# Kernel optimization log

Measured on AMD Instinct MI355X. Metric: run time of the kernel, lower is better.

Reference implementation:

```python
import jax, jax.numpy as jnp
import numpy as np

DN = ('NCHW', 'OIHW', 'NCHW')

def conv2d(x, w, b):
    y = jax.lax.conv_general_dilated(x, w, window_strides=(1, 1), padding='VALID', dimension_numbers=DN)
    return y + b[None, :, None, None]

def setup_inputs() -> dict:
    key = jax.random.key(0)
    ks = jax.random.split(key, 16)
    s = 0.02  # small init scale to keep relu chains numerically tame
    B, Cin, OUT = 128, 4, 9
    return {
        'state_m': jax.random.normal(ks[0], (B, Cin, 100, 100), jnp.float32),
        'state_g': jax.random.normal(ks[1], (B, 2), jnp.float32),
        'state_v': jax.random.normal(ks[2], (B, 2), jnp.float32),
        'conv1_w': jax.random.normal(ks[3], (32, Cin, 32, 32), jnp.float32) * s,
        'conv1_b': jnp.zeros((32,), jnp.float32),
        'conv2_w': jax.random.normal(ks[4], (64, 32, 32, 32), jnp.float32) * s,
        'conv2_b': jnp.zeros((64,), jnp.float32),
        'conv3_w': jax.random.normal(ks[5], (64, 64, 8, 8), jnp.float32) * s,
        'conv3_b': jnp.zeros((64,), jnp.float32),
        'conv4_w': jax.random.normal(ks[6], (64, 64, 8, 8), jnp.float32) * s,
        'conv4_b': jnp.zeros((64,), jnp.float32),
        'fc1_w': jax.random.normal(ks[7], (67, 4), jnp.float32) * s,
        'fc1_b': jnp.zeros((67,), jnp.float32),
        'fc2_w': jax.random.normal(ks[8], (512, 6400), jnp.float32) * s,
        'fc2_b': jnp.zeros((512,), jnp.float32),
        'fc3_w': jax.random.normal(ks[9], (512, 512), jnp.float32) * s,
        'fc3_b': jnp.zeros((512,), jnp.float32),
        'fc4_ea_w': jax.random.normal(ks[10], (OUT, 512), jnp.float32) * s,
        'fc4_ea_b': jnp.zeros((OUT,), jnp.float32),
        'fc4_ev_w': jax.random.normal(ks[11], (1, 512), jnp.float32) * s,
        'fc4_ev_b': jnp.zeros((1,), jnp.float32),
    }

def reference(state_m, state_g, state_v,
              conv1_w, conv1_b, conv2_w, conv2_b, conv3_w, conv3_b, conv4_w, conv4_b,
              fc1_w, fc1_b, fc2_w, fc2_b, fc3_w, fc3_b,
              fc4_ea_w, fc4_ea_b, fc4_ev_w, fc4_ev_b):
    x_m = jax.nn.relu(conv2d(state_m, conv1_w, conv1_b))   # [B,32,69,69]
    x_m = jax.nn.relu(conv2d(x_m, conv2_w, conv2_b))       # [B,64,38,38]
    x_m = jax.nn.relu(conv2d(x_m, conv3_w, conv3_b))       # [B,64,31,31]
    x_gv_ = jax.nn.relu(jnp.concatenate([state_g, state_v], axis=1) @ fc1_w.T + fc1_b)  # [B,67]
    convw = x_m.shape[2]  # 31
    # Torch loop overwrites x_gv each iteration: final tile is filled with x_gv_[0, convw-1]
    scalar = x_gv_[0, convw - 1]
    x_pls = x_m + scalar  # broadcast add (the CPU round-trip tile in torch)
    x_pls = jax.nn.relu(conv2d(x_pls, conv4_w, conv4_b))   # [B,64,24,24]
    x_pls = jax.nn.relu(conv2d(x_pls, conv4_w, conv4_b))   # [B,64,17,17]
    x_pls = jax.nn.relu(conv2d(x_pls, conv4_w, conv4_b))   # [B,64,10,10]
    x = x_pls.reshape(x_pls.shape[0], -1)                  # [B,6400]
    x = jax.nn.relu(x @ fc2_w.T + fc2_b)
    x = jax.nn.relu(x @ fc3_w.T + fc3_b)
    adv = x @ fc4_ea_w.T + fc4_ea_b                        # [B,outputs]
    val = x @ fc4_ev_w.T + fc4_ev_b                        # [B,1]
    return adv + val - jnp.mean(adv, axis=1, keepdims=True)
```

## Files before the change

kernel.cpp:

```cpp
#include <hip/hip_runtime.h>
#include <stdint.h>


using bf16_t = __bf16;
using bf16x8 = __attribute__((ext_vector_type(8))) __bf16;
using bf16x4 = __attribute__((ext_vector_type(4))) __bf16;
using f32x4  = __attribute__((ext_vector_type(4))) float;
using f32x16 = __attribute__((ext_vector_type(16))) float;

__device__ __forceinline__ f32x4 mfma16(bf16x8 a, bf16x8 b, f32x4 c) {
    return __builtin_amdgcn_mfma_f32_16x16x32_bf16(a, b, c, 0, 0, 0);
}
__device__ __forceinline__ f32x16 mfma32(bf16x8 a, bf16x8 b, f32x16 c) {
    return __builtin_amdgcn_mfma_f32_32x32x16_bf16(a, b, c, 0, 0, 0);
}

template<bool A16>
__device__ __forceinline__ bf16x8 load_frag(const bf16_t* p) {
    if constexpr (A16) {
        return *reinterpret_cast<const bf16x8*>(p);
    } else {
        union { bf16x8 v; uint64_t u[2]; } r;
        r.u[0] = *reinterpret_cast<const uint64_t*>(p);
        r.u[1] = *reinterpret_cast<const uint64_t*>(p + 4);
        return r.v;
    }
}

template<int CIN>
__global__ void pack_w(const float* __restrict__ src, bf16_t* __restrict__ dst,
                       int COUT, int KK) {
    int total = COUT * KK;
    for (int t = blockIdx.x * blockDim.x + threadIdx.x; t < total;
         t += gridDim.x * blockDim.x) {
        int cout = t / KK;
        int khw  = t - cout * KK;
        alignas(16) bf16_t tmp[CIN];
        #pragma unroll
        for (int c = 0; c < CIN; ++c)
            tmp[c] = (bf16_t)src[((size_t)cout * CIN + c) * KK + khw];
        bf16_t* d = dst + (size_t)t * CIN;
        if constexpr (CIN == 1) {
            d[0] = tmp[0];
        } else if constexpr (CIN == 4) {
            *reinterpret_cast<uint2*>(d) = *reinterpret_cast<const uint2*>(tmp);
        } else {
            #pragma unroll
            for (int c = 0; c < CIN; c += 8)
                *reinterpret_cast<uint4*>(d + c) =
                    *reinterpret_cast<const uint4*>(tmp + c);
        }
    }
}

template<int CIN, int COUT, int K>
__global__ void pack_wA(const float* __restrict__ src, bf16_t* __restrict__ dst) {
    constexpr int S  = K * CIN / 16;
    constexpr int NT = COUT / 32;
    int t = blockIdx.x * 256 + threadIdx.x;
    int l  = t & 63;
    int f  = t >> 6;
    int n  = f % NT;
    int fs = f / NT;
    int s  = fs % S;
    int kh = fs / S;
    if (kh >= K) return;
    int cout = n * 32 + (l & 31);
    int k0   = s * 16 + (l >> 5) * 8;
    alignas(16) bf16_t tmp[8];
    #pragma unroll
    for (int e = 0; e < 8; ++e) {
        int k   = k0 + e;
        int kw  = k / CIN;
        int cin = k % CIN;
        tmp[e] = (bf16_t)src[(((size_t)cout * CIN + cin) * K + kh) * K + kw];
    }
    *reinterpret_cast<uint4*>(dst + (size_t)t * 8) =
        *reinterpret_cast<const uint4*>(tmp);
}

__global__ void fc1_scalar(const float* __restrict__ g, const float* __restrict__ v,
                           const float* __restrict__ w, const float* __restrict__ b,
                           float* __restrict__ outp) {
    if (threadIdx.x == 0 && blockIdx.x == 0) {
        float s = b[30] + g[0] * w[120] + g[1] * w[121] + v[0] * w[122] + v[1] * w[123];
        *outp = s > 0.f ? s : 0.f;
    }
}

__global__ __launch_bounds__(256, 2) void conv2_k4(
    const bf16_t* __restrict__ in, const bf16_t* __restrict__ wA,
    const float* __restrict__ bias, bf16_t* __restrict__ out) {
    constexpr int W = 69, OW = 38, CIN = 32;
    constexpr int P    = OW * OW;
    constexpr int ROWB = W * CIN * 2;
    constexpr int PS   = (W + 1) * 16;
    constexpr int SLOTB = 4576;
    constexpr int NSLOT = 16;
    constexpr int LDSB  = NSLOT * SLOTB;
    constexpr int S = 64, NT = 2, WMT = 3;
    constexpr int BPX = 384;
    constexpr int CHR = ROWB / 16;
    constexpr int CH4 = 4 * CHR;
    __shared__ __align__(16) char smem[LDSB];

    const int tid  = threadIdx.x;
    const int wave = tid >> 6, lane = tid & 63;
    const int l31  = lane & 31, h = lane >> 5;
    const int img  = blockIdx.z;
    const int p0   = blockIdx.x * BPX;

    const char* inb = (const char*)(in + (size_t)img * (W * W * CIN));
    const int r0 = p0 / OW;
    int plast = p0 + BPX - 1; if (plast > P - 1) plast = P - 1;
    const int r1 = plast / OW;

    int pix[WMT], ldsadr[WMT];
    #pragma unroll
    for (int m = 0; m < WMT; ++m) {
        int p  = p0 + (wave * WMT + m) * 32 + l31;
        pix[m] = p;
        int pc = p < P ? p : P - 1;
        int oh = pc / OW;
        int ow = pc - oh * OW;
        ldsadr[m] = (oh & 15) * SLOTB + ow * 16 + h * PS;
    }

    for (int r = r0; r <= r1 + 3; ++r) {
        const char* g = inb + (size_t)r * ROWB;
        int base = (r & 15) * SLOTB;
        for (int c = tid; c < CHR; c += 256)
            *reinterpret_cast<bf16x8*>(smem + base + (c & 3) * PS + (c >> 2) * 16) =
                *reinterpret_cast<const bf16x8*>(g + c * 16);
    }
    __syncthreads();

    f32x16 acc[WMT][NT] = {};
    int wsl = (r1 + 4) & 15;
    const char* gpre = inb + (size_t)(r1 + 4) * ROWB;
    const bf16_t* wl = wA + lane * 8;

    for (int kp = 0; kp < 8; ++kp) {
        const bool pf = kp < 7;
        bf16x8 stv[5];

#define STVISSUE                                                            \
        if (pf) {                                                           \
            _Pragma("unroll")                                               \
            for (int i = 0; i < 5; ++i) {                                   \
                int c = i * 256 + tid;                                      \
                if (c < CH4) stv[i] = *reinterpret_cast<const bf16x8*>(gpre + c * 16); \
            }                                                               \
        }

        #pragma unroll
        for (int kl = 0; kl < 4; ++kl) {
            const bf16_t* ap = wl + (size_t)(kp * 4 + kl) * (S * NT * 512);
            int adr[WMT];
            #pragma unroll
            for (int m = 0; m < WMT; ++m) {
                int a = ldsadr[m] + kl * SLOTB;
                adr[m] = a >= LDSB ? a - LDSB : a;
            }

            bf16x8 bS0[WMT], bS1[WMT], bS2[WMT], bS3[WMT];
            bf16x8 aS0[NT],  aS1[NT],  aS2[NT],  aS3[NT];

#define LOADSET(BS, AS, SIDX)                                               \
            {                                                               \
                const int _s = (SIDX);                                      \
                _Pragma("unroll")                                           \
                for (int m = 0; m < WMT; ++m)                               \
                    BS[m] = *reinterpret_cast<const bf16x8*>(                \
                        smem + adr[m] + (_s & 1) * (2 * PS) + (_s >> 1) * 16); \
                _Pragma("unroll")                                           \
                for (int n = 0; n < NT; ++n)                                \
                    AS[n] = *reinterpret_cast<const bf16x8*>(ap + (_s * NT + n) * 512); \
            }
#define MFMASET(BS, AS)                                                     \
            {                                                               \
                __builtin_amdgcn_s_setprio(1);                              \
                _Pragma("unroll")                                           \
                for (int m = 0; m < WMT; ++m)                               \
                    _Pragma("unroll")                                       \
                    for (int n = 0; n < NT; ++n)                            \
                        acc[m][n] = mfma32(AS[n], BS[m], acc[m][n]);        \
                __builtin_amdgcn_s_setprio(0);                              \
            }

            LOADSET(bS0, aS0, 0)
            LOADSET(bS1, aS1, 1)
            LOADSET(bS2, aS2, 2)
            MFMASET(bS0, aS0)  LOADSET(bS3, aS3, 3)
            MFMASET(bS1, aS1)  LOADSET(bS0, aS0, 4)
            MFMASET(bS2, aS2)  LOADSET(bS1, aS1, 5)
            MFMASET(bS3, aS3)  LOADSET(bS2, aS2, 6)
            if (kl == 0) { STVISSUE }
            for (int sb = 4; sb + 8 <= S; sb += 4) {
                MFMASET(bS0, aS0)  LOADSET(bS3, aS3, sb + 3)
                MFMASET(bS1, aS1)  LOADSET(bS0, aS0, sb + 4)
                MFMASET(bS2, aS2)  LOADSET(bS1, aS1, sb + 5)
                MFMASET(bS3, aS3)  LOADSET(bS2, aS2, sb + 6)
            }
            MFMASET(bS0, aS0)  LOADSET(bS3, aS3, S - 1)
            MFMASET(bS1, aS1)
            MFMASET(bS2, aS2)
            MFMASET(bS3, aS3)
#undef LOADSET
#undef MFMASET
        }
#undef STVISSUE

        if (pf) {
            #pragma unroll
            for (int i = 0; i < 5; ++i) {
                int c = i * 256 + tid;
                if (c < CH4) {
                    int j = c / CHR, u = c - j * CHR;
                    *reinterpret_cast<bf16x8*>(
                        smem + ((wsl + j) & 15) * SLOTB + (u & 3) * PS + (u >> 2) * 16) = stv[i];
                }
            }
            gpre += 4 * ROWB;
            wsl = (wsl + 4) & 15;
        }
        __syncthreads();
        #pragma unroll
        for (int m = 0; m < WMT; ++m) {
            int a2 = ldsadr[m] + 4 * SLOTB;
            ldsadr[m] = a2 >= LDSB ? a2 - LDSB : a2;
        }
    }

    bf16_t* outb = out + (size_t)img * ((size_t)P * 64);
    #pragma unroll
    for (int m = 0; m < WMT; ++m) {
        if (pix[m] < P) {
            #pragma unroll
            for (int n = 0; n < NT; ++n) {
                #pragma unroll
                for (int rg = 0; rg < 4; ++rg) {
                    int cb = n * 32 + rg * 8 + h * 4;
                    f32x4 bv = *reinterpret_cast<const f32x4*>(bias + cb);
                    union { bf16x4 v; uint2 u; } o;
                    #pragma unroll
                    for (int j = 0; j < 4; ++j) {
                        float x = acc[m][n][rg * 4 + j] + bv[j];
                        o.v[j] = (bf16_t)(x > 0.f ? x : 0.f);
                    }
                    *reinterpret_cast<uint2*>(outb + (size_t)pix[m] * 64 + cb) = o.u;
                }
            }
        }
    }
}

template<int CIN, int COUT, int W, int K, int OW, int WMT, int NSLOT,
         int ADD_SCALAR>
__global__ __launch_bounds__(256, 2) void conv_rr(
    const bf16_t* __restrict__ in, const bf16_t* __restrict__ wA,
    const float* __restrict__ bias, bf16_t* __restrict__ out,
    const float* __restrict__ scal) {
    constexpr int  P     = OW * OW;
    constexpr int  PIXB  = CIN * 2;
    constexpr int  ROWB  = W * PIXB;
    constexpr bool TR    = (CIN >= 16);
    constexpr int  NCH   = TR ? PIXB / 16 : 1;
    constexpr int  SPP   = TR ? NCH / 2 : 1;
    constexpr int  PS    = TR ? (W + 1) * 16 : 0;
    constexpr int  SLOTB0 = TR ? NCH * PS : ROWB;
    constexpr int  PADB  = TR ? ((16 * OW - SLOTB0) % 128 + 128) % 128 : 0;
    constexpr int  SLOTB = SLOTB0 + PADB;
    constexpr int  LDSB  = NSLOT * SLOTB;
    constexpr int  S     = K * CIN / 16;
    constexpr int  NT    = COUT / 32;
    constexpr int  BPX   = WMT * 32 * 4;
    constexpr int  CH    = ROWB / 16;
    constexpr int  NLD   = (CH + 255) / 256;
    __shared__ __align__(16) char smem[LDSB];

    const int tid  = threadIdx.x;
    const int wave = tid >> 6, lane = tid & 63;
    const int l31  = lane & 31, h = lane >> 5;
    const int img  = blockIdx.z;
    const int p0   = blockIdx.x * BPX;

    const char* inb = (const char*)(in + (size_t)img * ((size_t)W * W * CIN));

    const int r0 = p0 / OW;
    int plast = p0 + BPX - 1; if (plast > P - 1) plast = P - 1;
    const int r1 = plast / OW;

    int woff[NLD];
    #pragma unroll
    for (int i = 0; i < NLD; ++i) {
        int c = i * 256 + tid;
        if (c < CH) woff[i] = TR ? (c % NCH) * PS + (c / NCH) * 16 : c * 16;
        else        woff[i] = 0;
    }

    int pix[WMT], ldsadr[WMT];
    #pragma unroll
    for (int m = 0; m < WMT; ++m) {
        int p  = p0 + (wave * WMT + m) * 32 + l31;
        pix[m] = p;
        int pc = p < P ? p : P - 1;
        int oh = pc / OW;
        int ow = pc - oh * OW;
        ldsadr[m] = (oh % NSLOT) * SLOTB +
                    (TR ? ow * 16 + h * PS : ow * PIXB + h * 16);
    }

    for (int r = r0; r <= r1; ++r) {
        const char* g = inb + (size_t)r * ROWB;
        int base = (r % NSLOT) * SLOTB;
        for (int c = tid; c < CH; c += 256) {
            bf16x8 v = *reinterpret_cast<const bf16x8*>(g + c * 16);
            int off = TR ? (c % NCH) * PS + (c / NCH) * 16 : c * 16;
            *reinterpret_cast<bf16x8*>(smem + base + off) = v;
        }
    }
    __syncthreads();

    f32x16 acc[WMT][NT] = {};

    int wsl = (r1 + 1) % NSLOT;
    const char* gpre = inb + (size_t)(r1 + 1) * ROWB;
    const bf16_t* wl = wA + lane * 8;

    for (int kh = 0; kh < K; ++kh) {
        bf16x8 stv[NLD];
        const bool pf = kh < K - 1;
        const bf16_t* ap = wl + (size_t)kh * (S * NT * 512);

        auto bread = [&](int m, int s) -> bf16x8 {
            int a = TR ? ldsadr[m] + (s % SPP) * (2 * PS) + (s / SPP) * 16
                       : ldsadr[m] + s * 32;
            return *reinterpret_cast<const bf16x8*>(smem + a);
        };
        bf16x8 bcur[WMT], acur[NT];
        #pragma unroll
        for (int m = 0; m < WMT; ++m) bcur[m] = bread(m, 0);
        #pragma unroll
        for (int n = 0; n < NT; ++n)
            acur[n] = *reinterpret_cast<const bf16x8*>(ap + n * 512);

        #pragma unroll
        for (int s = 0; s < S - 1; ++s) {
            bf16x8 bnx[WMT], anx[NT];
            #pragma unroll
            for (int m = 0; m < WMT; ++m) bnx[m] = bread(m, s + 1);
            #pragma unroll
            for (int n = 0; n < NT; ++n)
                anx[n] = *reinterpret_cast<const bf16x8*>(ap + ((s + 1) * NT + n) * 512);
            if (s == 2 && pf) {
                #pragma unroll
                for (int i = 0; i < NLD; ++i) {
                    int c = i * 256 + tid;
                    if (c < CH) stv[i] = *reinterpret_cast<const bf16x8*>(gpre + c * 16);
                }
            }
            #pragma unroll
            for (int m = 0; m < WMT; ++m)
                #pragma unroll
                for (int n = 0; n < NT; ++n)
                    acc[m][n] = mfma32(acur[n], bcur[m], acc[m][n]);
            #pragma unroll
            for (int m = 0; m < WMT; ++m) bcur[m] = bnx[m];
            #pragma unroll
            for (int n = 0; n < NT; ++n) acur[n] = anx[n];
        }
        #pragma unroll
        for (int m = 0; m < WMT; ++m)
            #pragma unroll
            for (int n = 0; n < NT; ++n)
                acc[m][n] = mfma32(acur[n], bcur[m], acc[m][n]);

        if (pf) {
            int wb0 = wsl * SLOTB;
            #pragma unroll
            for (int i = 0; i < NLD; ++i) {
                int c = i * 256 + tid;
                if (c < CH)
                    *reinterpret_cast<bf16x8*>(smem + wb0 + woff[i]) = stv[i];
            }
            gpre += ROWB;
            wsl = (wsl + 1 == NSLOT) ? 0 : wsl + 1;
        }
        __syncthreads();
        #pragma unroll
        for (int m = 0; m < WMT; ++m) {
            int a2 = ldsadr[m] + SLOTB;
            ldsadr[m] = a2 >= LDSB ? a2 - LDSB : a2;
        }
    }

    float sc = 0.f;
    if constexpr (ADD_SCALAR) sc = *scal;
    bf16_t* outb = out + (size_t)img * ((size_t)P * COUT);
    #pragma unroll
    for (int m = 0; m < WMT; ++m) {
        if (pix[m] < P) {
            #pragma unroll
            for (int n = 0; n < NT; ++n) {
                #pragma unroll
                for (int rg = 0; rg < 4; ++rg) {
                    int cb = n * 32 + rg * 8 + h * 4;
                    f32x4 bv = *reinterpret_cast<const f32x4*>(bias + cb);
                    union { bf16x4 v; uint2 u; } o;
                    #pragma unroll
                    for (int j = 0; j < 4; ++j) {
                        float x = acc[m][n][rg * 4 + j] + bv[j];
                        x = x > 0.f ? x : 0.f;
                        x += sc;
                        o.v[j] = (bf16_t)x;
                    }
                    *reinterpret_cast<uint2*>(outb + (size_t)pix[m] * COUT + cb) = o.u;
                }
            }
        }
    }
}

template<int CIN, int COUT, int W, int K, int OW, int NBLK, int WMT,
         int ADD_SCALAR, bool A16>
__global__ __launch_bounds__(256, 2) void conv_mfma(
    const bf16_t* __restrict__ in, const bf16_t* __restrict__ wp,
    const float* __restrict__ bias, bf16_t* __restrict__ out,
    const float* __restrict__ scal) {
    constexpr int P    = OW * OW;
    constexpr int KCIN = K * CIN;
    constexpr int KTOT = K * KCIN;
    constexpr int RS   = KCIN / 32;
    constexpr int NT   = NBLK / 16;
    constexpr int BMT  = WMT * 4;

    const int b     = blockIdx.z;
    const int cout0 = blockIdx.y * NBLK;
    const int wave  = threadIdx.x >> 6;
    const int lane  = threadIdx.x & 63;
    const int l15   = lane & 15;
    const int l4    = lane >> 4;
    const int mt0   = blockIdx.x * BMT + wave * WMT;

    const bf16_t* inb = in + (size_t)b * (W * W * CIN);

    int      pix[WMT];
    uint32_t pb[WMT];
    #pragma unroll
    for (int m = 0; m < WMT; ++m) {
        int p  = (mt0 + m) * 16 + l15;
        pix[m] = p;
        int pc = p < P ? p : P - 1;
        int oh = pc / OW;
        int ow = pc - oh * OW;
        pb[m]  = (uint32_t)(oh * W + ow) * CIN;
    }
    uint32_t wb[NT];
    #pragma unroll
    for (int n = 0; n < NT; ++n)
        wb[n] = (uint32_t)(cout0 + n * 16 + l15) * KTOT + (uint32_t)l4 * 8u;

    f32x4 acc[WMT][NT];
    #pragma unroll
    for (int m = 0; m < WMT; ++m)
        #pragma unroll
        for (int n = 0; n < NT; ++n)
            acc[m][n] = f32x4{0.f, 0.f, 0.f, 0.f};

    uint32_t bofs = (uint32_t)l4 * 8u;
    for (int kh = 0; kh < K; ++kh) {
        #pragma unroll
        for (int s = 0; s < RS; ++s) {
            bf16x8 af[NT];
            #pragma unroll
            for (int n = 0; n < NT; ++n)
                af[n] = load_frag<true>(wp + wb[n] + kh * KCIN + s * 32);
            #pragma unroll
            for (int m = 0; m < WMT; ++m) {
                bf16x8 bfr = load_frag<A16>(inb + pb[m] + bofs + s * 32);
                #pragma unroll
                for (int n = 0; n < NT; ++n)
                    acc[m][n] = mfma16(af[n], bfr, acc[m][n]);
            }
        }
        bofs += (uint32_t)(W * CIN);
    }

    float sc = 0.f;
    if constexpr (ADD_SCALAR) sc = *scal;
    bf16_t* outb = out + (size_t)b * P * COUT;
    #pragma unroll
    for (int n = 0; n < NT; ++n) {
        const int cb = cout0 + n * 16 + l4 * 4;
        f32x4 bv = *reinterpret_cast<const f32x4*>(bias + cb);
        #pragma unroll
        for (int m = 0; m < WMT; ++m) {
            if (pix[m] < P) {
                f32x4 v = acc[m][n];
                union { bf16x4 h; uint2 u; } st;
                #pragma unroll
                for (int r = 0; r < 4; ++r) {
                    float x = v[r] + bv[r];
                    x = x > 0.f ? x : 0.f;
                    x += sc;
                    st.h[r] = (bf16_t)x;
                }
                *reinterpret_cast<uint2*>(outb + (size_t)pix[m] * COUT + cb) = st.u;
            }
        }
    }
}

__global__ __launch_bounds__(256, 2) void fc2_kernel(
    const bf16_t* __restrict__ x, const bf16_t* __restrict__ w,
    float* __restrict__ part) {
    const int nb = blockIdx.x, kc = blockIdx.y;
    const int wave = threadIdx.x >> 6, lane = threadIdx.x & 63;
    const int l15 = lane & 15, l4 = lane >> 4;
    const int wm = wave & 1, wn = wave >> 1;

    f32x4 acc[4][2];
    #pragma unroll
    for (int m = 0; m < 4; ++m)
        #pragma unroll
        for (int n = 0; n < 2; ++n) acc[m][n] = f32x4{0.f, 0.f, 0.f, 0.f};

    uint32_t xb[4], wbf[2];
    #pragma unroll
    for (int m = 0; m < 4; ++m)
        xb[m] = (uint32_t)(16 * (wm * 4 + m) + l15) * 6400u + kc * 1600u + l4 * 8u;
    #pragma unroll
    for (int n = 0; n < 2; ++n)
        wbf[n] = (uint32_t)(nb * 64 + wn * 32 + n * 16 + l15) * 6400u + kc * 1600u + l4 * 8u;

    for (int s = 0; s < 50; ++s) {
        bf16x8 af[2];
        #pragma unroll
        for (int n = 0; n < 2; ++n)
            af[n] = load_frag<true>(w + wbf[n] + s * 32);
        #pragma unroll
        for (int m = 0; m < 4; ++m) {
            bf16x8 bfr = load_frag<true>(x + xb[m] + s * 32);
            #pragma unroll
            for (int n = 0; n < 2; ++n)
                acc[m][n] = mfma16(af[n], bfr, acc[m][n]);
        }
    }
    #pragma unroll
    for (int m = 0; m < 4; ++m) {
        int bcol = 16 * (wm * 4 + m) + l15;
        #pragma unroll
        for (int n = 0; n < 2; ++n) {
            int cf = nb * 64 + wn * 32 + n * 16 + l4 * 4;
            *reinterpret_cast<f32x4*>(part + ((size_t)kc * 128 + bcol) * 512 + cf) =
                acc[m][n];
        }
    }
}

__global__ void fc2_reduce(const float* __restrict__ part,
                           const float* __restrict__ bias,
                           bf16_t* __restrict__ xo) {
    int t = blockIdx.x * 256 + threadIdx.x;
    if (t < 128 * 512) {
        int b = t >> 9, co = t & 511;
        float s = bias[co];
        #pragma unroll
        for (int kc = 0; kc < 4; ++kc) s += part[((size_t)kc * 128 + b) * 512 + co];
        xo[t] = (bf16_t)(s > 0.f ? s : 0.f);
    }
}

__global__ __launch_bounds__(256, 2) void fc3_kernel(
    const bf16_t* __restrict__ x, const bf16_t* __restrict__ w,
    const float* __restrict__ bias, bf16_t* __restrict__ xo) {
    const int nb = blockIdx.x;
    const int wave = threadIdx.x >> 6, lane = threadIdx.x & 63;
    const int l15 = lane & 15, l4 = lane >> 4;

    f32x4 acc[2][4];
    #pragma unroll
    for (int m = 0; m < 2; ++m)
        #pragma unroll
        for (int n = 0; n < 4; ++n) acc[m][n] = f32x4{0.f, 0.f, 0.f, 0.f};

    uint32_t xb[2], wbf[4];
    #pragma unroll
    for (int m = 0; m < 2; ++m)
        xb[m] = (uint32_t)(16 * (wave * 2 + m) + l15) * 512u + l4 * 8u;
    #pragma unroll
    for (int n = 0; n < 4; ++n)
        wbf[n] = (uint32_t)(nb * 64 + n * 16 + l15) * 512u + l4 * 8u;

    #pragma unroll
    for (int s = 0; s < 16; ++s) {
        bf16x8 af[4];
        #pragma unroll
        for (int n = 0; n < 4; ++n) af[n] = load_frag<true>(w + wbf[n] + s * 32);
        #pragma unroll
        for (int m = 0; m < 2; ++m) {
            bf16x8 bfr = load_frag<true>(x + xb[m] + s * 32);
            #pragma unroll
            for (int n = 0; n < 4; ++n)
                acc[m][n] = mfma16(af[n], bfr, acc[m][n]);
        }
    }
    #pragma unroll
    for (int n = 0; n < 4; ++n) {
        int cf = nb * 64 + n * 16 + l4 * 4;
        f32x4 bv = *reinterpret_cast<const f32x4*>(bias + cf);
        #pragma unroll
        for (int m = 0; m < 2; ++m) {
            int brow = 16 * (wave * 2 + m) + l15;
            union { bf16x4 h; uint2 u; } st;
            #pragma unroll
            for (int r = 0; r < 4; ++r) {
                float v = acc[m][n][r] + bv[r];
                st.h[r] = (bf16_t)(v > 0.f ? v : 0.f);
            }
            *reinterpret_cast<uint2*>(xo + (size_t)brow * 512 + cf) = st.u;
        }
    }
}

__global__ void final_kernel(const bf16_t* __restrict__ x,
                             const float* __restrict__ eaw, const float* __restrict__ eab,
                             const float* __restrict__ evw, const float* __restrict__ evb,
                             float* __restrict__ out) {
    int b = blockIdx.x, lane = threadIdx.x;
    bf16x8 xv = *reinterpret_cast<const bf16x8*>(x + (size_t)b * 512 + lane * 8);
    float xs[8];
    #pragma unroll
    for (int i = 0; i < 8; ++i) xs[i] = (float)xv[i];
    float a[10];
    #pragma unroll
    for (int j = 0; j < 10; ++j) {
        const float* wr = (j < 9) ? (eaw + (size_t)j * 512) : evw;
        const f32x4* w4 = reinterpret_cast<const f32x4*>(wr + lane * 8);
        f32x4 w0 = w4[0], w1 = w4[1];
        float s = 0.f;
        #pragma unroll
        for (int i = 0; i < 4; ++i) s += xs[i] * w0[i];
        #pragma unroll
        for (int i = 0; i < 4; ++i) s += xs[4 + i] * w1[i];
        a[j] = s;
    }
    #pragma unroll
    for (int off = 1; off < 64; off <<= 1)
        #pragma unroll
        for (int j = 0; j < 10; ++j) a[j] += __shfl_xor(a[j], off);
    if (lane < 9) {
        float val  = a[9] + evb[0];
        float mean = 0.f;
        #pragma unroll
        for (int j = 0; j < 9; ++j) mean += a[j] + eab[j];
        mean *= (1.f / 9.f);
        out[b * 9 + lane] = a[lane] + eab[lane] + val - mean;
    }
}

extern "C" void kernel_launch(void* const* d_in, const int* in_sizes, int n_in,
                              void* d_out, int out_size, void* d_ws, size_t ws_size,
                              hipStream_t stream) {
    const float* state_m  = (const float*)d_in[0];
    const float* state_g  = (const float*)d_in[1];
    const float* state_v  = (const float*)d_in[2];
    const float* conv1_w  = (const float*)d_in[3];
    const float* conv1_b  = (const float*)d_in[4];
    const float* conv2_w  = (const float*)d_in[5];
    const float* conv2_b  = (const float*)d_in[6];
    const float* conv3_w  = (const float*)d_in[7];
    const float* conv3_b  = (const float*)d_in[8];
    const float* conv4_w  = (const float*)d_in[9];
    const float* conv4_b  = (const float*)d_in[10];
    const float* fc1_w    = (const float*)d_in[11];
    const float* fc1_b    = (const float*)d_in[12];
    const float* fc2_w    = (const float*)d_in[13];
    const float* fc2_b    = (const float*)d_in[14];
    const float* fc3_w    = (const float*)d_in[15];
    const float* fc3_b    = (const float*)d_in[16];
    const float* fc4_ea_w = (const float*)d_in[17];
    const float* fc4_ea_b = (const float*)d_in[18];
    const float* fc4_ev_w = (const float*)d_in[19];
    const float* fc4_ev_b = (const float*)d_in[20];

    char* ws = (char*)d_ws;
    bf16_t* w1A    = (bf16_t*)(ws + 0);
    bf16_t* w2A    = (bf16_t*)(ws + 262144);
    bf16_t* w3A    = (bf16_t*)(ws + 4456448);
    bf16_t* w4A    = (bf16_t*)(ws + 4980736);
    bf16_t* w4p    = (bf16_t*)(ws + 5505024);
    bf16_t* fc2wp  = (bf16_t*)(ws + 6029312);
    bf16_t* fc3wp  = (bf16_t*)(ws + 12582912);
    float*  scal   = (float*) (ws + 13107200);
    float*  part   = (float*) (ws + 13107456);
    bf16_t* x2fc   = (bf16_t*)(ws + 14156032);
    bf16_t* x3fc   = (bf16_t*)(ws + 14287104);
    bf16_t* a0     = (bf16_t*)(ws + 14418176);
    bf16_t* x4a    = (bf16_t*)(ws + 14418176);
    bf16_t* x1     = (bf16_t*)(ws + 24658176);
    bf16_t* x4b    = (bf16_t*)(ws + 24658176);
    bf16_t* x4c    = (bf16_t*)(ws + 29393152);
    bf16_t* x2     = (bf16_t*)(ws + 63660288);
    bf16_t* x3     = (bf16_t*)(ws + 87318784);
    (void)in_sizes; (void)n_in; (void)out_size; (void)ws_size;

    pack_wA<4, 32, 32> <<<dim3(64),   256, 0, stream>>>(conv1_w, w1A);
    pack_wA<32, 64, 32><<<dim3(1024), 256, 0, stream>>>(conv2_w, w2A);
    pack_wA<64, 64, 8> <<<dim3(128),  256, 0, stream>>>(conv3_w, w3A);
    pack_wA<64, 64, 8> <<<dim3(128),  256, 0, stream>>>(conv4_w, w4A);
    pack_w<64><<<dim3(16),   256, 0, stream>>>(conv4_w, w4p, 64, 64);
    pack_w<64><<<dim3(200),  256, 0, stream>>>(fc2_w, fc2wp, 512, 100);
    pack_w<1> <<<dim3(1024), 256, 0, stream>>>(fc3_w, fc3wp, 512, 512);
    pack_w<4> <<<dim3(1024), 256, 0, stream>>>(state_m, a0, 128, 10000);
    fc1_scalar<<<1, 64, 0, stream>>>(state_g, state_v, fc1_w, fc1_b, scal);

    conv_rr<4, 32, 100, 32, 69, 3, 8, 0>
        <<<dim3(13, 1, 128), 256, 0, stream>>>(a0, w1A, conv1_b, x1, nullptr);
    conv2_k4<<<dim3(4, 1, 128), 256, 0, stream>>>(x1, w2A, conv2_b, x2);
    conv_rr<64, 64, 38, 8, 31, 2, 11, 1>
        <<<dim3(4, 1, 128), 256, 0, stream>>>(x2, w3A, conv3_b, x3, scal);
    conv_rr<64, 64, 31, 8, 24, 2, 13, 0>
        <<<dim3(3, 1, 128), 256, 0, stream>>>(x3, w4A, conv4_b, x4a, nullptr);
    conv_rr<64, 64, 24, 8, 17, 2, 17, 0>
        <<<dim3(2, 1, 128), 256, 0, stream>>>(x4a, w4A, conv4_b, x4b, nullptr);
    conv_mfma<64, 64, 17, 8, 10, 32, 1, 0, true>
        <<<dim3(2, 2, 128), 256, 0, stream>>>(x4b, w4p, conv4_b, x4c, nullptr);

    fc2_kernel<<<dim3(8, 4), 256, 0, stream>>>(x4c, fc2wp, part);
    fc2_reduce<<<dim3(256), 256, 0, stream>>>(part, fc2_b, x2fc);
    fc3_kernel<<<dim3(8), 256, 0, stream>>>(x2fc, fc3wp, fc3_b, x3fc);
    final_kernel<<<dim3(128), 64, 0, stream>>>(x3fc, fc4_ea_w, fc4_ea_b,
                                               fc4_ev_w, fc4_ev_b, (float*)d_out);
}
```

Measured before the change: 1.146 ms.

## Generalize conv2 k4 pipelined kernel and apply it to conv1 with retuned slots

```diff
diff --git a/kernel.cpp b/kernel.cpp
--- a/kernel.cpp
+++ b/kernel.cpp
@@ -88,20 +88,26 @@
     }
 }
 
-__global__ __launch_bounds__(256, 2) void conv2_k4(
+template<int CIN, int COUT, int W, int K, int OW, int WMT, int NSLOT,
+         int PS_, int SLOTB_>
+__global__ __launch_bounds__(256, 2) void conv_k4(
     const bf16_t* __restrict__ in, const bf16_t* __restrict__ wA,
     const float* __restrict__ bias, bf16_t* __restrict__ out) {
-    constexpr int W = 69, OW = 38, CIN = 32;
-    constexpr int P    = OW * OW;
-    constexpr int ROWB = W * CIN * 2;
-    constexpr int PS   = (W + 1) * 16;
-    constexpr int SLOTB = 4576;
-    constexpr int NSLOT = 16;
-    constexpr int LDSB  = NSLOT * SLOTB;
-    constexpr int S = 64, NT = 2, WMT = 3;
-    constexpr int BPX = 384;
-    constexpr int CHR = ROWB / 16;
-    constexpr int CH4 = 4 * CHR;
+    constexpr int  P     = OW * OW;
+    constexpr int  PIXB  = CIN * 2;
+    constexpr int  ROWB  = W * PIXB;
+    constexpr bool TR    = (CIN >= 16);
+    constexpr int  NCH   = TR ? PIXB / 16 : 1;
+    constexpr int  PS    = PS_;
+    constexpr int  SLOTB = SLOTB_;
+    constexpr int  LDSB  = NSLOT * SLOTB;
+    constexpr int  S     = K * CIN / 16;
+    constexpr int  NT    = COUT / 32;
+    constexpr int  BPX   = WMT * 32 * 4;
+    constexpr int  CHR   = ROWB / 16;
+    constexpr int  CH4   = 4 * CHR;
+    constexpr int  NLD   = (CH4 + 255) / 256;
+    constexpr int  KP    = K / 4;
     __shared__ __align__(16) char smem[LDSB];
 
     const int tid  = threadIdx.x;
@@ -110,7 +116,7 @@
     const int img  = blockIdx.z;
     const int p0   = blockIdx.x * BPX;
 
-    const char* inb = (const char*)(in + (size_t)img * (W * W * CIN));
+    const char* inb = (const char*)(in + (size_t)img * ((size_t)W * W * CIN));
     const int r0 = p0 / OW;
     int plast = p0 + BPX - 1; if (plast > P - 1) plast = P - 1;
     const int r1 = plast / OW;
@@ -123,31 +129,34 @@
         int pc = p < P ? p : P - 1;
         int oh = pc / OW;
         int ow = pc - oh * OW;
-        ldsadr[m] = (oh & 15) * SLOTB + ow * 16 + h * PS;
+        ldsadr[m] = (oh % NSLOT) * SLOTB +
+                    (TR ? ow * 16 + h * PS : ow * PIXB + h * 16);
     }
 
     for (int r = r0; r <= r1 + 3; ++r) {
         const char* g = inb + (size_t)r * ROWB;
-        int base = (r & 15) * SLOTB;
-        for (int c = tid; c < CHR; c += 256)
-            *reinterpret_cast<bf16x8*>(smem + base + (c & 3) * PS + (c >> 2) * 16) =
+        int base = (r % NSLOT) * SLOTB;
+        for (int c = tid; c < CHR; c += 256) {
+            int off = TR ? (c % NCH) * PS + (c / NCH) * 16 : c * 16;
+            *reinterpret_cast<bf16x8*>(smem + base + off) =
                 *reinterpret_cast<const bf16x8*>(g + c * 16);
+        }
     }
     __syncthreads();
 
     f32x16 acc[WMT][NT] = {};
-    int wsl = (r1 + 4) & 15;
+    int wsl = (r1 + 4) % NSLOT;
     const char* gpre = inb + (size_t)(r1 + 4) * ROWB;
     const bf16_t* wl = wA + lane * 8;
 
-    for (int kp = 0; kp < 8; ++kp) {
-        const bool pf = kp < 7;
-        bf16x8 stv[5];
+    for (int kp = 0; kp < KP; ++kp) {
+        const bool pf = kp < KP - 1;
+        bf16x8 stv[NLD];
 
 #define STVISSUE                                                            \
         if (pf) {                                                           \
             _Pragma("unroll")                                               \
-            for (int i = 0; i < 5; ++i) {                                   \
+            for (int i = 0; i < NLD; ++i) {                                 \
                 int c = i * 256 + tid;                                      \
                 if (c < CH4) stv[i] = *reinterpret_cast<const bf16x8*>(gpre + c * 16); \
             }                                                               \
@@ -170,9 +179,11 @@
             {                                                               \
                 const int _s = (SIDX);                                      \
                 _Pragma("unroll")                                           \
-                for (int m = 0; m < WMT; ++m)                               \
-                    BS[m] = *reinterpret_cast<const bf16x8*>(                \
-                        smem + adr[m] + (_s & 1) * (2 * PS) + (_s >> 1) * 16); \
+                for (int m = 0; m < WMT; ++m) {                             \
+                    int a = TR ? adr[m] + (_s & 1) * (2 * PS) + (_s >> 1) * 16 \
+                               : adr[m] + _s * 32;                          \
+                    BS[m] = *reinterpret_cast<const bf16x8*>(smem + a);     \
+                }                                                           \
                 _Pragma("unroll")                                           \
                 for (int n = 0; n < NT; ++n)                                \
                     AS[n] = *reinterpret_cast<const bf16x8*>(ap + (_s * NT + n) * 512); \
@@ -213,16 +224,17 @@
 
         if (pf) {
             #pragma unroll
-            for (int i = 0; i < 5; ++i) {
+            for (int i = 0; i < NLD; ++i) {
                 int c = i * 256 + tid;
                 if (c < CH4) {
                     int j = c / CHR, u = c - j * CHR;
-                    *reinterpret_cast<bf16x8*>(
-                        smem + ((wsl + j) & 15) * SLOTB + (u & 3) * PS + (u >> 2) * 16) = stv[i];
+                    int sl = wsl + j; if (sl >= NSLOT) sl -= NSLOT;
+                    int off = TR ? (u % NCH) * PS + (u / NCH) * 16 : u * 16;
+                    *reinterpret_cast<bf16x8*>(smem + sl * SLOTB + off) = stv[i];
                 }
             }
-            gpre += 4 * ROWB;
-            wsl = (wsl + 4) & 15;
+            gpre += 4 * (size_t)ROWB;
+            wsl += 4; if (wsl >= NSLOT) wsl -= NSLOT;
         }
         __syncthreads();
         #pragma unroll
@@ -232,7 +244,7 @@
         }
     }
 
-    bf16_t* outb = out + (size_t)img * ((size_t)P * 64);
+    bf16_t* outb = out + (size_t)img * ((size_t)P * COUT);
     #pragma unroll
     for (int m = 0; m < WMT; ++m) {
         if (pix[m] < P) {
@@ -248,7 +260,7 @@
                         float x = acc[m][n][rg * 4 + j] + bv[j];
                         o.v[j] = (bf16_t)(x > 0.f ? x : 0.f);
                     }
-                    *reinterpret_cast<uint2*>(outb + (size_t)pix[m] * 64 + cb) = o.u;
+                    *reinterpret_cast<uint2*>(outb + (size_t)pix[m] * COUT + cb) = o.u;
                 }
             }
         }
@@ -716,9 +728,10 @@
     pack_w<4> <<<dim3(1024), 256, 0, stream>>>(state_m, a0, 128, 10000);
     fc1_scalar<<<1, 64, 0, stream>>>(state_g, state_v, fc1_w, fc1_b, scal);
 
-    conv_rr<4, 32, 100, 32, 69, 3, 8, 0>
-        <<<dim3(13, 1, 128), 256, 0, stream>>>(a0, w1A, conv1_b, x1, nullptr);
-    conv2_k4<<<dim3(4, 1, 128), 256, 0, stream>>>(x1, w2A, conv2_b, x2);
+    conv_k4<4, 32, 100, 32, 69, 3, 14, 0, 800>
+        <<<dim3(13, 1, 128), 256, 0, stream>>>(a0, w1A, conv1_b, x1);
+    conv_k4<32, 64, 69, 32, 38, 3, 18, 1104, 4448>
+        <<<dim3(4, 1, 128), 256, 0, stream>>>(x1, w2A, conv2_b, x2);
     conv_rr<64, 64, 38, 8, 31, 2, 11, 1>
         <<<dim3(4, 1, 128), 256, 0, stream>>>(x2, w3A, conv3_b, x3, scal);
     conv_rr<64, 64, 31, 8, 24, 2, 13, 0>
```

Result: slower. 1.219 ms (+6.4%).
